# Performance work log

Measured on AMD Instinct MI355X. Metric: run time of the kernel, lower is better.

## Reference

```python
import jax, jax.numpy as jnp
import numpy as np

PARA_CH = 256
FEATURE_CH = 256
PI = 3.14159  # matches the literal in the torch source


def _linear_params(key, fan_in, fan_out):
    kw, kb = jax.random.split(key)
    bound = 1.0 / np.sqrt(fan_in)
    W = jax.random.uniform(kw, (fan_in, fan_out), minval=-bound, maxval=bound, dtype=jnp.float32)
    b = jax.random.uniform(kb, (fan_out,), minval=-bound, maxval=bound, dtype=jnp.float32)
    return W, b


def setup_inputs() -> dict:
    key = jax.random.key(0)
    ks = jax.random.split(key, 6)
    feature_map = jax.random.normal(ks[0], (4, FEATURE_CH, 128, 128), dtype=jnp.float32)
    para_code = jax.random.normal(ks[1], (4, PARA_CH), dtype=jnp.float32)
    W1, b1 = _linear_params(ks[2], PARA_CH, PARA_CH)
    Ws, bs = _linear_params(ks[3], PARA_CH, FEATURE_CH)
    Wr, br = _linear_params(ks[4], PARA_CH, FEATURE_CH)
    Wt, bt = _linear_params(ks[5], PARA_CH, 2 * FEATURE_CH)
    return {"feature_map": feature_map, "para_code": para_code,
            "W1": W1, "b1": b1, "Ws": Ws, "bs": bs,
            "Wr": Wr, "br": br, "Wt": Wt, "bt": bt}


def _coord_1d(n):
    # align_corners=True-style normalized coordinates, as in make_coordinate_grid_3d
    return 2.0 * (jnp.arange(n, dtype=jnp.float32) / (n - 1)) - 1.0


def _trilinear_sample_zeros(vol, gx, gy, gz):
    """F.grid_sample 5D equivalent: mode='bilinear' (trilinear), padding_mode='zeros',
    align_corners=False. vol: [B,D,H,W] (channel dim of size 1 squeezed out);
    gx,gy,gz: [B,Do,Ho,Wo] normalized coords. Returns [B,Do,Ho,Wo]."""
    B, D, H, W = vol.shape
    ix = ((gx + 1.0) * W - 1.0) * 0.5
    iy = ((gy + 1.0) * H - 1.0) * 0.5
    iz = ((gz + 1.0) * D - 1.0) * 0.5
    x0f, y0f, z0f = jnp.floor(ix), jnp.floor(iy), jnp.floor(iz)
    wx, wy, wz = ix - x0f, iy - y0f, iz - z0f
    x0 = x0f.astype(jnp.int32); x1 = x0 + 1
    y0 = y0f.astype(jnp.int32); y1 = y0 + 1
    z0 = z0f.astype(jnp.int32); z1 = z0 + 1
    vflat = vol.reshape(B, -1)

    def gather(zi, yi, xi):
        valid = (zi >= 0) & (zi < D) & (yi >= 0) & (yi < H) & (xi >= 0) & (xi < W)
        zc = jnp.clip(zi, 0, D - 1)
        yc = jnp.clip(yi, 0, H - 1)
        xc = jnp.clip(xi, 0, W - 1)
        flat = (zc * H + yc) * W + xc  # [B,Do,Ho,Wo]
        v = jnp.take_along_axis(vflat, flat.reshape(B, -1), axis=1).reshape(flat.shape)
        return jnp.where(valid, v, 0.0)

    out = (gather(z0, y0, x0) * (1 - wz) * (1 - wy) * (1 - wx)
           + gather(z0, y0, x1) * (1 - wz) * (1 - wy) * wx
           + gather(z0, y1, x0) * (1 - wz) * wy * (1 - wx)
           + gather(z0, y1, x1) * (1 - wz) * wy * wx
           + gather(z1, y0, x0) * wz * (1 - wy) * (1 - wx)
           + gather(z1, y0, x1) * wz * (1 - wy) * wx
           + gather(z1, y1, x0) * wz * wy * (1 - wx)
           + gather(z1, y1, x1) * wz * wy * wx)
    return out


def reference(feature_map, para_code, W1, b1, Ws, bs, Wr, br, Wt, bt):
    B, C, H, W = feature_map.shape  # C == feature_ch == depth of 3D grid
    p = jax.nn.relu(para_code @ W1 + b1)                      # [B, para_ch]
    scale = jax.nn.sigmoid(p @ Ws + bs) * 2.0                 # [B, C]
    angle = jnp.tanh(p @ Wr + br) * PI                        # [B, C]
    translation = jnp.tanh(p @ Wt + bt).reshape(B, C, 2)      # [B, C, 2]
    ca, sa = jnp.cos(angle), jnp.sin(angle)
    # rotation matrix [[cos, -sin], [sin, cos]] per (batch, channel)
    rot = jnp.stack([jnp.stack([ca, -sa], -1), jnp.stack([sa, ca], -1)], -2)  # [B,C,2,2]

    x = _coord_1d(W)  # [W]
    y = _coord_1d(H)  # [H]
    z = _coord_1d(C)  # [C] (depth == channel dim)
    grid_xy = jnp.stack(jnp.broadcast_arrays(x[None, None, :], y[None, :, None]), -1)  # [1,H,W,2] -> broadcast to [C,H,W,2]
    grid_xy = jnp.broadcast_to(grid_xy, (C, H, W, 2))

    # per-pixel affine transform: rot @ [x,y] * scale + trans
    trans_grid = jnp.einsum('bcij,chwj->bchwi', rot, grid_xy)
    trans_grid = trans_grid * scale[:, :, None, None, None] + translation[:, :, None, None, :]
    gx = trans_grid[..., 0]
    gy = trans_grid[..., 1]
    gz = jnp.broadcast_to(z[None, :, None, None], (B, C, H, W))

    return _trilinear_sample_zeros(feature_map, gx, gy, gz)  # [B,C,H,W]
```

## Files before the change

kernel.cpp:

```cpp
#include <hip/hip_runtime.h>
#include <math.h>

#define BATCH 4
#define CH    256
#define HH    128
#define WW    128
#define PC    256
#define PI_F  3.14159f
#define PLANE (HH * WW)
#define NP    4

__global__ __launch_bounds__(1024)
void adaat_params_kernel(const float* __restrict__ pc,
                         const float* __restrict__ W1, const float* __restrict__ b1,
                         const float* __restrict__ Ws, const float* __restrict__ bs,
                         const float* __restrict__ Wr, const float* __restrict__ br,
                         const float* __restrict__ Wt, const float* __restrict__ bt,
                         float4* __restrict__ params) {
    __shared__ float red[1024];
    __shared__ float p_sh[PC];
    __shared__ float hd[4][PC];
    const int b = blockIdx.x;
    const int t = threadIdx.x;

    {
        const int jj = t & 255, kk = t >> 8;
        const float* pcb = pc + b * PC + kk * 64;
        const float* w   = W1 + (kk * 64) * PC + jj;
        float acc = 0.0f;
#pragma unroll 8
        for (int i = 0; i < 64; ++i)
            acc = fmaf(pcb[i], w[i * PC], acc);
        red[t] = acc;
    }
    __syncthreads();
    if (t < 256)
        p_sh[t] = fmaxf(red[t] + red[256 + t] + red[512 + t] + red[768 + t] + b1[t], 0.0f);
    __syncthreads();

    {
        const int c = t & 255, h = t >> 8;
        const float* wp; int stride;
        if      (h == 0) { wp = Ws + c;               stride = PC;     }
        else if (h == 1) { wp = Wr + c;               stride = PC;     }
        else             { wp = Wt + 2 * c + (h == 3); stride = 2 * PC; }
        float dot = 0.0f;
#pragma unroll 8
        for (int k = 0; k < PC; ++k)
            dot = fmaf(p_sh[k], wp[(size_t)k * stride], dot);
        hd[h][c] = dot;
    }
    __syncthreads();
    if (t < 256) {
        const int c = t;
        const float s   = 2.0f / (1.0f + expf(-(hd[0][c] + bs[c])));
        const float ang = tanhf(hd[1][c] + br[c]) * PI_F;
        float sa, ca;
        sincosf(ang, &sa, &ca);
        const float A  = s * ca, B = s * sa;
        const float Tx = tanhf(hd[2][c] + bt[2 * c]);
        const float Ty = tanhf(hd[3][c] + bt[2 * c + 1]);
        params[b * CH + c] = make_float4(A * (128.0f / 127.0f),
                                         B * (128.0f / 127.0f),
                                         64.0f * (Tx - A + B) + 63.5f,
                                         64.0f * (Ty - A - B) + 63.5f);
    }
}

struct Stage { float4 a[4]; float4 b[4]; };

__device__ __forceinline__ Stage stage_load(const float* __restrict__ pl0,
                                            const float* __restrict__ pl1, int t) {
    Stage s;
#pragma unroll
    for (int j = 0; j < 4; ++j) {
        const int f = 4 * (t + 1024 * j);
        s.a[j] = *(const float4*)(pl0 + f);
        s.b[j] = *(const float4*)(pl1 + f);
    }
    return s;
}

__device__ __forceinline__ void stage_store(float* __restrict__ buf, const Stage& s,
                                            float wz0, float wz1, int t) {
#pragma unroll
    for (int j = 0; j < 4; ++j) {
        const int f = 4 * (t + 1024 * j);
        const int y = f >> 7, x = f & (WW - 1);
        float4 c;
        c.x = fmaf(wz0, s.a[j].x, wz1 * s.b[j].x);
        c.y = fmaf(wz0, s.a[j].y, wz1 * s.b[j].y);
        c.z = fmaf(wz0, s.a[j].z, wz1 * s.b[j].z);
        c.w = fmaf(wz0, s.a[j].w, wz1 * s.b[j].w);
        *(float4*)&buf[y * WW + (x ^ ((y & 3) << 3))] = c;
    }
}

__device__ __forceinline__ void gather_plane(const float* __restrict__ buf,
                                             const float4 P,
                                             float* __restrict__ outp,
                                             const float yf, const int xi) {
    const float cA = P.x, cB = P.y, C0 = P.z, C1 = P.w;
#pragma unroll 2
    for (int k = 0; k < 16; ++k) {
        const float xf  = (float)(k * 8 + xi);
        const float ixf = fmaf(cA, xf, fmaf(-cB, yf, C0));
        const float iyf = fmaf(cB, xf, fmaf(cA, yf, C1));
        const float x0f = floorf(ixf);
        const float y0f = floorf(iyf);
        const float fx  = ixf - x0f;
        const float fy  = iyf - y0f;
        const float mx0 = (x0f >= 0.0f  && x0f < 128.0f) ? (1.0f - fx) : 0.0f;
        const float mx1 = (x0f >= -1.0f && x0f < 127.0f) ? fx          : 0.0f;
        const float my0 = (y0f >= 0.0f  && y0f < 128.0f) ? (1.0f - fy) : 0.0f;
        const float my1 = (y0f >= -1.0f && y0f < 127.0f) ? fy          : 0.0f;

        const int x0i = (int)x0f, y0i = (int)y0f;
        const int xc0 = min(max(x0i,     0), WW - 1);
        const int xc1 = min(max(x0i + 1, 0), WW - 1);
        const int yc0 = min(max(y0i,     0), HH - 1);
        const int yc1 = min(max(y0i + 1, 0), HH - 1);

        const int r0 = yc0 * WW, r1 = yc1 * WW;
        const int s0 = (yc0 & 3) << 3, s1 = (yc1 & 3) << 3;
        const float v00 = buf[r0 + (xc0 ^ s0)];
        const float v01 = buf[r0 + (xc1 ^ s0)];
        const float v10 = buf[r1 + (xc0 ^ s1)];
        const float v11 = buf[r1 + (xc1 ^ s1)];

        outp[k * 8 + xi] = my0 * (mx0 * v00 + mx1 * v01)
                         + my1 * (mx0 * v10 + mx1 * v11);
    }
}

__global__ __launch_bounds__(1024, 4)
void adaat_sample_kernel(const float* __restrict__ fm,
                         const float4* __restrict__ params,
                         float* __restrict__ out) {
    __shared__ float buf[2][PLANE];

    const int t   = threadIdx.x;
    const int bc0 = blockIdx.x * NP;
    const int b   = bc0 >> 8;
    const int wv  = t >> 6, l = t & 63;
    const int xi  = l & 7;
    const int yj  = wv * 8 + (l >> 3);
    const float yf = (float)yj;

    const float* base = fm + (size_t)b * (CH * PLANE);

    const float* pl0[NP]; const float* pl1[NP];
    float w0[NP], w1[NP];
#pragma unroll
    for (int i = 0; i < NP; ++i) {
        const int   c   = (bc0 + i) & (CH - 1);
        const float iz  = (256.0f / 255.0f) * (float)c - 0.5f;
        const float zf  = floorf(iz);
        const float fz  = iz - zf;
        const int   z0  = (int)zf;
        w0[i]  = (z0 >= 0)     ? (1.0f - fz) : 0.0f;
        w1[i]  = (z0 + 1 < CH) ? fz          : 0.0f;
        pl0[i] = base + (size_t)max(z0, 0)          * PLANE;
        pl1[i] = base + (size_t)min(z0 + 1, CH - 1) * PLANE;
    }
    float4 Ps[NP];
#pragma unroll
    for (int i = 0; i < NP; ++i) Ps[i] = params[bc0 + i];

    Stage s = stage_load(pl0[0], pl1[0], t);
    stage_store(&buf[0][0], s, w0[0], w1[0], t);
    __syncthreads();

#pragma unroll
    for (int i = 1; i < NP; ++i) {
        s = stage_load(pl0[i], pl1[i], t);
        gather_plane(&buf[(i - 1) & 1][0], Ps[i - 1],
                     out + (size_t)(bc0 + i - 1) * PLANE + yj * WW, yf, xi);
        stage_store(&buf[i & 1][0], s, w0[i], w1[i], t);
        __syncthreads();
    }

    gather_plane(&buf[(NP - 1) & 1][0], Ps[NP - 1],
                 out + (size_t)(bc0 + NP - 1) * PLANE + yj * WW, yf, xi);
}

extern "C" void kernel_launch(void* const* d_in, const int* in_sizes, int n_in,
                              void* d_out, int out_size, void* d_ws, size_t ws_size,
                              hipStream_t stream) {
    const float* feature_map = (const float*)d_in[0];
    const float* para_code   = (const float*)d_in[1];
    const float* W1 = (const float*)d_in[2];
    const float* b1 = (const float*)d_in[3];
    const float* Ws = (const float*)d_in[4];
    const float* bs = (const float*)d_in[5];
    const float* Wr = (const float*)d_in[6];
    const float* br = (const float*)d_in[7];
    const float* Wt = (const float*)d_in[8];
    const float* bt = (const float*)d_in[9];

    float4* params = (float4*)d_ws;

    adaat_params_kernel<<<BATCH, 1024, 0, stream>>>(
        para_code, W1, b1, Ws, bs, Wr, br, Wt, bt, params);

    adaat_sample_kernel<<<BATCH * CH / NP, 1024, 0, stream>>>(
        feature_map, params, (float*)d_out);
}
```

Measured before the change: 172.5 us.

## Fuse parameter MLP into sampling kernel with per-block redundant head computation

New measurement: 157.7 us. -8.6%, faster.

```diff
diff --git a/kernel.cpp b/kernel.cpp
--- a/kernel.cpp
+++ b/kernel.cpp
@@ -10,61 +10,8 @@
 #define PLANE (HH * WW)
 #define NP    4
 
-__global__ __launch_bounds__(1024)
-void adaat_params_kernel(const float* __restrict__ pc,
-                         const float* __restrict__ W1, const float* __restrict__ b1,
-                         const float* __restrict__ Ws, const float* __restrict__ bs,
-                         const float* __restrict__ Wr, const float* __restrict__ br,
-                         const float* __restrict__ Wt, const float* __restrict__ bt,
-                         float4* __restrict__ params) {
-    __shared__ float red[1024];
-    __shared__ float p_sh[PC];
-    __shared__ float hd[4][PC];
-    const int b = blockIdx.x;
-    const int t = threadIdx.x;
-
-    {
-        const int jj = t & 255, kk = t >> 8;
-        const float* pcb = pc + b * PC + kk * 64;
-        const float* w   = W1 + (kk * 64) * PC + jj;
-        float acc = 0.0f;
-#pragma unroll 8
-        for (int i = 0; i < 64; ++i)
-            acc = fmaf(pcb[i], w[i * PC], acc);
-        red[t] = acc;
-    }
-    __syncthreads();
-    if (t < 256)
-        p_sh[t] = fmaxf(red[t] + red[256 + t] + red[512 + t] + red[768 + t] + b1[t], 0.0f);
-    __syncthreads();
-
-    {
-        const int c = t & 255, h = t >> 8;
-        const float* wp; int stride;
-        if      (h == 0) { wp = Ws + c;               stride = PC;     }
-        else if (h == 1) { wp = Wr + c;               stride = PC;     }
-        else             { wp = Wt + 2 * c + (h == 3); stride = 2 * PC; }
-        float dot = 0.0f;
-#pragma unroll 8
-        for (int k = 0; k < PC; ++k)
-            dot = fmaf(p_sh[k], wp[(size_t)k * stride], dot);
-        hd[h][c] = dot;
-    }
-    __syncthreads();
-    if (t < 256) {
-        const int c = t;
-        const float s   = 2.0f / (1.0f + expf(-(hd[0][c] + bs[c])));
-        const float ang = tanhf(hd[1][c] + br[c]) * PI_F;
-        float sa, ca;
-        sincosf(ang, &sa, &ca);
-        const float A  = s * ca, B = s * sa;
-        const float Tx = tanhf(hd[2][c] + bt[2 * c]);
-        const float Ty = tanhf(hd[3][c] + bt[2 * c + 1]);
-        params[b * CH + c] = make_float4(A * (128.0f / 127.0f),
-                                         B * (128.0f / 127.0f),
-                                         64.0f * (Tx - A + B) + 63.5f,
-                                         64.0f * (Ty - A - B) + 63.5f);
-    }
+__device__ __forceinline__ void barrier_lds() {
+    asm volatile("s_waitcnt lgkmcnt(0)\n\ts_barrier" ::: "memory");
 }
 
 struct Stage { float4 a[4]; float4 b[4]; };
@@ -100,12 +47,14 @@
                                              const float4 P,
                                              float* __restrict__ outp,
                                              const float yf, const int xi) {
-    const float cA = P.x, cB = P.y, C0 = P.z, C1 = P.w;
+    const float cA = P.x, cB = P.y;
+    const float Dx = fmaf(-P.y, yf, P.z);
+    const float Dy = fmaf( P.x, yf, P.w);
 #pragma unroll 2
     for (int k = 0; k < 16; ++k) {
         const float xf  = (float)(k * 8 + xi);
-        const float ixf = fmaf(cA, xf, fmaf(-cB, yf, C0));
-        const float iyf = fmaf(cB, xf, fmaf(cA, yf, C1));
+        const float ixf = fmaf(cA, xf, Dx);
+        const float iyf = fmaf(cB, xf, Dy);
         const float x0f = floorf(ixf);
         const float y0f = floorf(iyf);
         const float fx  = ixf - x0f;
@@ -134,53 +83,109 @@
 }
 
 __global__ __launch_bounds__(1024, 4)
-void adaat_sample_kernel(const float* __restrict__ fm,
-                         const float4* __restrict__ params,
-                         float* __restrict__ out) {
-    __shared__ float buf[2][PLANE];
+void adaat_fused_kernel(const float* __restrict__ fm,
+                        const float* __restrict__ pc,
+                        const float* __restrict__ W1, const float* __restrict__ b1,
+                        const float* __restrict__ Ws, const float* __restrict__ bs,
+                        const float* __restrict__ Wr, const float* __restrict__ br,
+                        const float* __restrict__ Wt, const float* __restrict__ bt,
+                        float* __restrict__ out) {
+    __shared__ float  buf[2][PLANE];
+    __shared__ float  p_sh[PC];
+    __shared__ float  sh_head[16];
+    __shared__ float4 sh_par[NP];
 
     const int t   = threadIdx.x;
     const int bc0 = blockIdx.x * NP;
     const int b   = bc0 >> 8;
-    const int wv  = t >> 6, l = t & 63;
-    const int xi  = l & 7;
-    const int yj  = wv * 8 + (l >> 3);
-    const float yf = (float)yj;
 
     const float* base = fm + (size_t)b * (CH * PLANE);
-
     const float* pl0[NP]; const float* pl1[NP];
     float w0[NP], w1[NP];
 #pragma unroll
     for (int i = 0; i < NP; ++i) {
-        const int   c   = (bc0 + i) & (CH - 1);
-        const float iz  = (256.0f / 255.0f) * (float)c - 0.5f;
-        const float zf  = floorf(iz);
-        const float fz  = iz - zf;
-        const int   z0  = (int)zf;
+        const int   c  = (bc0 + i) & (CH - 1);
+        const float iz = (256.0f / 255.0f) * (float)c - 0.5f;
+        const float zf = floorf(iz);
+        const float fz = iz - zf;
+        const int   z0 = (int)zf;
         w0[i]  = (z0 >= 0)     ? (1.0f - fz) : 0.0f;
         w1[i]  = (z0 + 1 < CH) ? fz          : 0.0f;
         pl0[i] = base + (size_t)max(z0, 0)          * PLANE;
         pl1[i] = base + (size_t)min(z0 + 1, CH - 1) * PLANE;
     }
-    float4 Ps[NP];
-#pragma unroll
-    for (int i = 0; i < NP; ++i) Ps[i] = params[bc0 + i];
 
     Stage s = stage_load(pl0[0], pl1[0], t);
+
+    {
+        float* red = &buf[1][0];
+        const int jj = t & 255, kk = t >> 8;
+        const float* pcb = pc + b * PC + kk * 64;
+        const float* w   = W1 + (kk * 64) * PC + jj;
+        float acc = 0.0f;
+#pragma unroll 8
+        for (int i = 0; i < 64; ++i)
+            acc = fmaf(pcb[i], w[i * PC], acc);
+        red[t] = acc;
+        barrier_lds();
+        if (t < 256)
+            p_sh[t] = fmaxf(red[t] + red[256 + t] + red[512 + t] + red[768 + t] + b1[t], 0.0f);
+        barrier_lds();
+    }
+
+    const int wv = t >> 6, l = t & 63;
+    {
+        const int q  = wv >> 2;
+        const int h  = wv & 3;
+        const int cq = (bc0 + q) & (CH - 1);
+        const float* wp; int stride;
+        if      (h == 0) { wp = Ws + cq;                stride = PC;     }
+        else if (h == 1) { wp = Wr + cq;                stride = PC;     }
+        else             { wp = Wt + 2 * cq + (h == 3); stride = 2 * PC; }
+        float dot = 0.0f;
+#pragma unroll
+        for (int m = 0; m < 4; ++m) {
+            const int k = l + 64 * m;
+            dot = fmaf(p_sh[k], wp[(size_t)k * stride], dot);
+        }
+#pragma unroll
+        for (int off = 32; off >= 1; off >>= 1)
+            dot += __shfl_xor(dot, off, 64);
+        if (l == 0) sh_head[wv] = dot;
+    }
+    barrier_lds();
+
+    if (t < NP) {
+        const int cq = (bc0 + t) & (CH - 1);
+        const float s2  = 2.0f / (1.0f + expf(-(sh_head[4 * t] + bs[cq])));
+        const float ang = tanhf(sh_head[4 * t + 1] + br[cq]) * PI_F;
+        float sa, ca;
+        sincosf(ang, &sa, &ca);
+        const float A  = s2 * ca, B = s2 * sa;
+        const float Tx = tanhf(sh_head[4 * t + 2] + bt[2 * cq]);
+        const float Ty = tanhf(sh_head[4 * t + 3] + bt[2 * cq + 1]);
+        sh_par[t] = make_float4(A * (128.0f / 127.0f),
+                                B * (128.0f / 127.0f),
+                                64.0f * (Tx - A + B) + 63.5f,
+                                64.0f * (Ty - A - B) + 63.5f);
+    }
+
     stage_store(&buf[0][0], s, w0[0], w1[0], t);
-    __syncthreads();
+    barrier_lds();
+
+    const int   xi = l & 7;
+    const int   yj = wv * 8 + (l >> 3);
+    const float yf = (float)yj;
 
 #pragma unroll
     for (int i = 1; i < NP; ++i) {
         s = stage_load(pl0[i], pl1[i], t);
-        gather_plane(&buf[(i - 1) & 1][0], Ps[i - 1],
+        gather_plane(&buf[(i - 1) & 1][0], sh_par[i - 1],
                      out + (size_t)(bc0 + i - 1) * PLANE + yj * WW, yf, xi);
         stage_store(&buf[i & 1][0], s, w0[i], w1[i], t);
-        __syncthreads();
-    }
-
-    gather_plane(&buf[(NP - 1) & 1][0], Ps[NP - 1],
+        barrier_lds();
+    }
+    gather_plane(&buf[(NP - 1) & 1][0], sh_par[NP - 1],
                  out + (size_t)(bc0 + NP - 1) * PLANE + yj * WW, yf, xi);
 }
 
@@ -198,11 +203,6 @@
     const float* Wt = (const float*)d_in[8];
     const float* bt = (const float*)d_in[9];
 
-    float4* params = (float4*)d_ws;
-
-    adaat_params_kernel<<<BATCH, 1024, 0, stream>>>(
-        para_code, W1, b1, Ws, bs, Wr, br, Wt, bt, params);
-
-    adaat_sample_kernel<<<BATCH * CH / NP, 1024, 0, stream>>>(
-        feature_map, params, (float*)d_out);
-}
+    adaat_fused_kernel<<<BATCH * CH / NP, 1024, 0, stream>>>(
+        feature_map, para_code, W1, b1, Ws, bs, Wr, br, Wt, bt, (float*)d_out);
+}
```
